# Kernel tuning notes

Hardware: AMD Instinct MI355X
Metric: run time of the kernel (lower is better)

Reference implementation:

```python
import jax, jax.numpy as jnp
from jax import lax
import numpy as np

EPS = 1e-5
SCALE, K_UP = 2, 5  # CARAFE defaults


def conv(x, w, pad=0):
    return lax.conv_general_dilated(x, w, (1, 1), [(pad, pad), (pad, pad)],
                                    dimension_numbers=('NCHW', 'OIHW', 'NCHW'))


def bn(x, g, b, m, v):
    # eval-mode BatchNorm2d
    inv = g * lax.rsqrt(v + EPS)
    return x * inv[None, :, None, None] + (b - m * inv)[None, :, None, None]


def carafe(X, comp_w, comp_g, comp_bt, comp_m, comp_v, enc_w, enc_g, enc_bt, enc_m, enc_v):
    b, c, h, w = X.shape
    k2 = K_UP * K_UP
    W = jax.nn.relu(bn(conv(X, comp_w), comp_g, comp_bt, comp_m, comp_v))  # (b, c_mid, h, w)
    W = bn(conv(W, enc_w, pad=1), enc_g, enc_bt, enc_m, enc_v)             # (b, k2*SCALE^2, h, w)
    # PixelShuffle(SCALE): (b, k2*r^2, h, w) -> (b, k2, h*r, w*r)
    W = W.reshape(b, k2, SCALE, SCALE, h, w).transpose(0, 1, 4, 2, 5, 3)
    W = W.reshape(b, k2, h * SCALE, w * SCALE)
    W = jax.nn.softmax(W, axis=1)
    # nearest upsample by SCALE
    Xu = jnp.repeat(jnp.repeat(X, SCALE, axis=2), SCALE, axis=3)
    pad = (K_UP // 2) * SCALE
    Xp = jnp.pad(Xu, ((0, 0), (0, 0), (pad, pad), (pad, pad)))
    h_, w_ = h * SCALE, w * SCALE
    # Unfold(kernel=K_UP, dilation=SCALE): channel-major then kernel index, matching torch
    patches = jnp.stack([Xp[:, :, i * SCALE:i * SCALE + h_, j * SCALE:j * SCALE + w_]
                         for i in range(K_UP) for j in range(K_UP)], axis=2)  # (b,c,k2,h_,w_)
    return jnp.einsum('bkhw,bckhw->bchw', W, patches)


def setup_inputs():
    key = jax.random.key(0)
    ks = iter(jax.random.split(key, 80))
    nk = lambda: next(ks)
    P = lambda shape, s=0.05: jax.random.normal(nk(), shape, jnp.float32) * s
    d = {}
    B, C_out = 4, 64
    cins = [128, 256, 512]
    hw = [(96, 160), (48, 80), (24, 40)]
    for i, (ci, (h, w)) in enumerate(zip(cins, hw)):
        d[f'x{i}'] = jax.random.normal(nk(), (B, ci, h, w), jnp.float32)
        d[f'lat{i}_w'] = P((C_out, ci, 1, 1))
        d[f'lat{i}_b'] = P((C_out,))
        d[f'fpn{i}_w'] = P((C_out, C_out, 3, 3))
        d[f'fpn{i}_b'] = P((C_out,))
    k2s2 = (SCALE * K_UP) ** 2
    for u in range(2):
        d[f'u{u}_comp_w'] = P((C_out, C_out, 1, 1))
        d[f'u{u}_enc_w'] = P((k2s2, C_out, 3, 3))
        for nm, c in [('comp', C_out), ('enc', k2s2)]:
            d[f'u{u}_{nm}_g'] = 1.0 + P((c,))
            d[f'u{u}_{nm}_bt'] = P((c,))
            d[f'u{u}_{nm}_m'] = P((c,))
            d[f'u{u}_{nm}_v'] = jax.random.uniform(nk(), (c,), jnp.float32, 0.5, 1.5)
    return d


def reference(x0, x1, x2,
              lat0_w, lat0_b, fpn0_w, fpn0_b,
              lat1_w, lat1_b, fpn1_w, fpn1_b,
              lat2_w, lat2_b, fpn2_w, fpn2_b,
              u0_comp_w, u0_enc_w, u0_comp_g, u0_comp_bt, u0_comp_m, u0_comp_v,
              u0_enc_g, u0_enc_bt, u0_enc_m, u0_enc_v,
              u1_comp_w, u1_enc_w, u1_comp_g, u1_comp_bt, u1_comp_m, u1_comp_v,
              u1_enc_g, u1_enc_bt, u1_enc_m, u1_enc_v):
    lat = [conv(x, w) + b[None, :, None, None] for x, w, b in
           [(x0, lat0_w, lat0_b), (x1, lat1_w, lat1_b), (x2, lat2_w, lat2_b)]]
    # top-down pathway with CARAFE upsampling
    lat[1] = lat[1] + carafe(lat[2], u1_comp_w, u1_comp_g, u1_comp_bt, u1_comp_m, u1_comp_v,
                             u1_enc_w, u1_enc_g, u1_enc_bt, u1_enc_m, u1_enc_v)
    lat[0] = lat[0] + carafe(lat[1], u0_comp_w, u0_comp_g, u0_comp_bt, u0_comp_m, u0_comp_v,
                             u0_enc_w, u0_enc_g, u0_enc_bt, u0_enc_m, u0_enc_v)
    outs = tuple(conv(l, w, pad=1) + b[None, :, None, None] for l, w, b in
                 [(lat[0], fpn0_w, fpn0_b), (lat[1], fpn1_w, fpn1_b), (lat[2], fpn2_w, fpn2_b)])
    return outs
```

## Files before the change

kernel.cpp:

```cpp
#include <hip/hip_runtime.h>

#define BN_EPS 1e-5f

typedef __attribute__((ext_vector_type(8))) short bf16x8;
typedef __attribute__((ext_vector_type(4))) float f32x4;

__device__ __forceinline__ unsigned short f2bf(float f) {
    unsigned u = __float_as_uint(f);
    return (unsigned short)((u + 0x7fffu + ((u >> 16) & 1u)) >> 16);
}
__device__ __forceinline__ unsigned packbf(float lo, float hi) {
    return ((unsigned)f2bf(hi) << 16) | (unsigned)f2bf(lo);
}

__global__ __launch_bounds__(256)
void prep_weights(const float* __restrict__ w0, const float* __restrict__ w1,
                  const float* __restrict__ w2, const float* __restrict__ w3,
                  const float* __restrict__ w4, unsigned short* __restrict__ dst,
                  const float* __restrict__ v0, const float* __restrict__ v1,
                  const float* __restrict__ v2, const float* __restrict__ v3,
                  const float* __restrict__ v4, unsigned short* __restrict__ dst1)
{
    int z = blockIdx.y;
    int i = blockIdx.x * 256 + threadIdx.x;
    if (z < 5) {
        const float* src; unsigned short* d; int C_out, COP;
        if (z < 3) {
            COP = 64; C_out = 64;
            src = (z == 0) ? w0 : (z == 1 ? w1 : w2);
            d = dst + z * 36864;
            if (i >= 36864) return;
        } else {
            COP = 112; C_out = 100;
            src = (z == 3) ? w3 : w4;
            d = dst + 110592 + (z - 3) * 64512;
            if (i >= 64512) return;
        }
        int tap = i / (COP * 64);
        int rem = i - tap * (COP * 64);
        int co = rem >> 6, ci = rem & 63;
        float v = (co < C_out) ? src[((size_t)co * 64 + ci) * 9 + tap] : 0.f;
        d[i] = f2bf(v);
    } else {
        int zz = z - 5;
        const float* s; int n; int off;
        if (zz == 0)      { s = v0; n = 8192;  off = 0; }
        else if (zz == 1) { s = v1; n = 16384; off = 8192; }
        else if (zz == 2) { s = v2; n = 32768; off = 24576; }
        else if (zz == 3) { s = v3; n = 4096;  off = 57344; }
        else              { s = v4; n = 4096;  off = 61440; }
        if (i >= n) return;
        dst1[off + i] = f2bf(s[i]);
    }
}

template<int COP, int CSPLIT, int MODE>
__device__ __forceinline__
void conv3x3_body(int rem, int TX, unsigned short* xs,
                  const unsigned* __restrict__ xp,
                  const unsigned short* __restrict__ wt,
                  const float* __restrict__ p0, const float* __restrict__ p1,
                  const float* __restrict__ p2, const float* __restrict__ p3,
                  float* __restrict__ out, int H, int W, int C_out)
{
    constexpr int NP = 324;
    constexpr int CT = COP / 16;
    static_assert(CT == CSPLIT, "CPB must be 1 (R1/R2 VGPR cliff)");

    int cs = rem % CSPLIT;
    int b  = (rem / CSPLIT) & 3;
    int t  = rem / (CSPLIT * 4);
    int x0 = (t % TX) * 16, y0 = (t / TX) * 16;

    int tid  = threadIdx.x;
    int lane = tid & 63, wid = tid >> 6;
    int lrow = lane >> 4, lcol = lane & 15;
    int HWp = H * W;

    int co0 = cs * 16;
    bool colok = (x0 + lcol) < W;

    f32x4 accA[2], accB[2];
#pragma unroll
    for (int rr = 0; rr < 2; ++rr) {
        accA[rr] = (f32x4){0.f, 0.f, 0.f, 0.f};
        accB[rr] = (f32x4){0.f, 0.f, 0.f, 0.f};
    }

    unsigned int* wsl = (unsigned int*)xs;

#pragma unroll 1
    for (int kb = 0; kb < 2; ++kb) {
        if (kb) __syncthreads();
        for (int p = tid; p < NP; p += 256) {
            int py = p / 18, px = p - py * 18;
            int gy = y0 + py - 1, gx = x0 + px - 1;
            bool ok = (gy >= 0) && (gy < H) && (gx >= 0) && (gx < W);
            const unsigned* gpp = xp + ((size_t)b * 32 + kb * 16) * HWp
                                     + (size_t)gy * W + gx;
#pragma unroll 8
            for (int cp = 0; cp < 16; ++cp) {
                unsigned pk = ok ? gpp[(size_t)cp * HWp] : 0u;
                wsl[((cp >> 2) * NP + p) * 4 + (cp & 3)] = pk;
            }
        }
        __syncthreads();

        bf16x8 a[9];
        const unsigned short* wl = wt + ((size_t)co0 + lcol) * 64 + kb * 32 + lrow * 8;
#pragma unroll
        for (int t9 = 0; t9 < 9; ++t9)
            a[t9] = *(const bf16x8*)(wl + (size_t)t9 * COP * 64);

#pragma unroll
        for (int rr = 0; rr < 2; ++rr) {
            int r0 = wid + rr * 8;
#pragma unroll
            for (int t9 = 0; t9 < 9; ++t9) {
                int dy = t9 / 3, dx = t9 - dy * 3;
                int g0 = lrow * NP + (r0 + dy) * 18 + lcol + dx;
                bf16x8 b0 = *(const bf16x8*)(xs + (size_t)g0 * 8);
                accA[rr] = __builtin_amdgcn_mfma_f32_16x16x32_bf16(a[t9], b0, accA[rr], 0, 0, 0);
                bf16x8 b1 = *(const bf16x8*)(xs + ((size_t)g0 + 4 * 18) * 8);
                accB[rr] = __builtin_amdgcn_mfma_f32_16x16x32_bf16(a[t9], b1, accB[rr], 0, 0, 0);
            }
        }
    }

    float sc[4], sh[4];
#pragma unroll
    for (int rg = 0; rg < 4; ++rg) {
        int co = co0 + lrow * 4 + rg;
        int cc = (co < C_out) ? co : 0;
        if (MODE == 0) { sc[rg] = 1.f; sh[rg] = p0[cc]; }
        else {
            float inv = p0[cc] * rsqrtf(p3[cc] + BN_EPS);
            sc[rg] = inv; sh[rg] = p1[cc] - p2[cc] * inv;
        }
    }
#pragma unroll
    for (int rr = 0; rr < 2; ++rr) {
        int r0 = wid + rr * 8;
        int yA = y0 + r0, yB = y0 + r0 + 4;
#pragma unroll
        for (int rg = 0; rg < 4; ++rg) {
            int co = co0 + lrow * 4 + rg;
            if (colok && co < C_out) {
                float* oc = out + (((size_t)b * C_out + co) * H) * W + x0 + lcol;
                if (yA < H) oc[(size_t)yA * W] = accA[rr][rg] * sc[rg] + sh[rg];
                if (yB < H) oc[(size_t)yB * W] = accB[rr][rg] * sc[rg] + sh[rg];
            }
        }
    }
}

__global__ __launch_bounds__(256, 6)
void enc_fpn(int encBlocks,
             const unsigned* __restrict__ cxp, const unsigned short* __restrict__ wt_e,
             const float* __restrict__ g, const float* __restrict__ bt,
             const float* __restrict__ m, const float* __restrict__ v,
             float* __restrict__ enc_out, int He, int We, int TXe,
             const unsigned* __restrict__ xp, const unsigned short* __restrict__ wt_f,
             const float* __restrict__ bias, float* __restrict__ fout,
             int Hf, int Wf, int TXf)
{
    __shared__ unsigned short xs[4 * 324 * 8];
    int f = blockIdx.x;
    if (f < encBlocks)
        conv3x3_body<112, 7, 1>(f, TXe, xs, cxp, wt_e,
                                g, bt, m, v, enc_out, He, We, 100);
    else
        conv3x3_body<64, 4, 0>(f - encBlocks, TXf, xs, xp, wt_f,
                               bias, nullptr, nullptr, nullptr, fout, Hf, Wf, 64);
}

__global__ __launch_bounds__(256, 6)
void fpn_multi(const unsigned* __restrict__ l0p, const unsigned short* __restrict__ wt0,
               const float* __restrict__ b0, float* __restrict__ o0)
{
    __shared__ unsigned short xs[4 * 324 * 8];
    conv3x3_body<64, 4, 0>(blockIdx.x, 10, xs, l0p, wt0,
                           b0, nullptr, nullptr, nullptr, o0, 96, 160, 64);
}

template<int C_IN, int NPX, int MODE, bool INPK, bool OUTMIR>
__device__ __forceinline__
void conv1x1_body(int f, unsigned short* xs,
                  const float* __restrict__ x, const unsigned* __restrict__ xp,
                  const unsigned short* __restrict__ wb,
                  const float* __restrict__ p0, const float* __restrict__ p1,
                  const float* __restrict__ p2, const float* __restrict__ p3,
                  float* __restrict__ out, unsigned* __restrict__ outp, int HW)
{
    constexpr int NT = NPX / 16;
    constexpr int QUADS = NPX / 4;
    int nb = HW / NPX;
    int px0 = (f % nb) * NPX;
    int b   = f / nb;

    int tid = threadIdx.x;
    int lane = tid & 63, wid = tid >> 6;
    int lrow = lane >> 4, lcol = lane & 15;
    const float*    xb  = INPK ? nullptr : x + (size_t)b * C_IN * HW + px0;
    const unsigned* xpb = INPK ? xp + (size_t)b * (C_IN / 2) * HW + px0 : nullptr;

    f32x4 acc[NT];
#pragma unroll
    for (int nt = 0; nt < NT; ++nt) acc[nt] = (f32x4){0.f, 0.f, 0.f, 0.f};

    for (int cc = 0; cc < C_IN; cc += 32) {
        if (cc) __syncthreads();
        for (int j = tid; j < 16 * QUADS; j += 256) {
            int q  = j & (QUADS - 1);
            int cp = j / QUADS;
            int px = q * 4;
            unsigned* wv = (unsigned*)xs + ((size_t)(cp >> 2) * NPX + px) * 4 + (cp & 3);
            if (INPK) {
                uint4 v = *(const uint4*)(xpb + (size_t)(cc / 2 + cp) * HW + px);
                wv[0] = v.x; wv[4] = v.y; wv[8] = v.z; wv[12] = v.w;
            } else {
                const float* s0 = xb + (size_t)(cc + 2 * cp) * HW + px;
                float4 v0 = *(const float4*)s0;
                float4 v1 = *(const float4*)(s0 + HW);
                wv[0]  = packbf(v0.x, v1.x);
                wv[4]  = packbf(v0.y, v1.y);
                wv[8]  = packbf(v0.z, v1.z);
                wv[12] = packbf(v0.w, v1.w);
            }
        }
        __syncthreads();

        bf16x8 a = *(const bf16x8*)(wb + (size_t)(wid * 16 + lcol) * C_IN + cc + lrow * 8);
#pragma unroll
        for (int nt = 0; nt < NT; ++nt) {
            bf16x8 bf = *(const bf16x8*)(xs + ((size_t)lrow * NPX + nt * 16 + lcol) * 8);
            acc[nt] = __builtin_amdgcn_mfma_f32_16x16x32_bf16(a, bf, acc[nt], 0, 0, 0);
        }
    }

    if (OUTMIR) {
#pragma unroll
        for (int rg = 0; rg < 4; rg += 2) {
            int co = wid * 16 + lrow * 4 + rg;
            float s0, h0, s1, h1;
            if (MODE == 0) { s0 = 1.f; h0 = p0[co]; s1 = 1.f; h1 = p0[co + 1]; }
            else {
                s0 = p0[co] * rsqrtf(p3[co] + BN_EPS);
                h0 = p1[co] - p2[co] * s0;
                s1 = p0[co + 1] * rsqrtf(p3[co + 1] + BN_EPS);
                h1 = p1[co + 1] - p2[co + 1] * s1;
            }
            unsigned* pp = outp + ((size_t)(b * 32 + (co >> 1))) * HW + px0;
#pragma unroll
            for (int nt = 0; nt < NT; ++nt) {
                float r0 = acc[nt][rg] * s0 + h0;
                float r1 = acc[nt][rg + 1] * s1 + h1;
                if (MODE == 1) { r0 = fmaxf(r0, 0.f); r1 = fmaxf(r1, 0.f); }
                pp[nt * 16 + lcol] = packbf(r0, r1);
            }
        }
    } else {
#pragma unroll
        for (int rg = 0; rg < 4; ++rg) {
            int co = wid * 16 + lrow * 4 + rg;
            float scale, shift;
            if (MODE == 0) { scale = 1.f; shift = p0[co]; }
            else {
                float inv = p0[co] * rsqrtf(p3[co] + BN_EPS);
                scale = inv; shift = p1[co] - p2[co] * inv;
            }
            float* op = out + ((size_t)(b * 64 + co)) * HW + px0;
#pragma unroll
            for (int nt = 0; nt < NT; ++nt) {
                float r = acc[nt][rg] * scale + shift;
                if (MODE == 1) r = fmaxf(r, 0.f);
                op[nt * 16 + lcol] = r;
            }
        }
    }
}

template<int C_IN, int NPX, int MODE, bool INPK, bool OUTMIR>
__global__ __launch_bounds__(256, 4)
void conv1x1_mfma(const float* __restrict__ x, const unsigned* __restrict__ xp,
                  const unsigned short* __restrict__ wb,
                  const float* __restrict__ p0, const float* __restrict__ p1,
                  const float* __restrict__ p2, const float* __restrict__ p3,
                  float* __restrict__ out, unsigned* __restrict__ outp, int HW)
{
    __shared__ __align__(16) unsigned short xs[4 * NPX * 8];
    int nb = HW / NPX;
    int f = blockIdx.x + nb * blockIdx.z;
    conv1x1_body<C_IN, NPX, MODE, INPK, OUTMIR>(f, xs, x, xp, wb, p0, p1, p2, p3, out, outp, HW);
}

__global__ __launch_bounds__(256, 4)
void lat_multi(const float* __restrict__ x0, const unsigned short* __restrict__ w0,
               const float* __restrict__ b0, float* __restrict__ lat0,
               const float* __restrict__ x1, const unsigned short* __restrict__ w1,
               const float* __restrict__ b1, float* __restrict__ lat1,
               const float* __restrict__ x2, const unsigned short* __restrict__ w2,
               const float* __restrict__ b2, unsigned* __restrict__ lat2p)
{
    __shared__ __align__(16) unsigned short xs[4 * 128 * 8];
    int f = blockIdx.x;
    if (f < 480)
        conv1x1_body<128, 128, 0, false, false>(f, xs, x0, nullptr, w0,
            b0, nullptr, nullptr, nullptr, lat0, nullptr, 15360);
    else if (f < 600)
        conv1x1_body<256, 128, 0, false, false>(f - 480, xs, x1, nullptr, w1,
            b1, nullptr, nullptr, nullptr, lat1, nullptr, 3840);
    else
        conv1x1_body<512, 64, 0, false, true>(f - 600, xs, x2, nullptr, w2,
            b2, nullptr, nullptr, nullptr, nullptr, lat2p, 960);
}

template<int CGS>
__global__ __launch_bounds__(256, 4)
void carafe_kernel(const unsigned* __restrict__ srcp, const float* __restrict__ logits,
                   const float* __restrict__ base, unsigned* __restrict__ dstp,
                   int h, int w)
{
    constexpr int SW = 12, NPX = 144;
    constexpr int CH = 64 / CGS;
    constexpr int CP = CH / 2;
    constexpr int CS = CH + 4;
    __shared__ float ls[NPX * CS];

    int tid = threadIdx.x;
    int x0 = blockIdx.x * 16, y0 = blockIdx.y * 16;
    int b  = blockIdx.z / CGS;
    int cs = blockIdx.z % CGS;
    int H = 2 * h, W = 2 * w;
    int xs0 = (x0 >> 1) - 2, ys0 = (y0 >> 1) - 2;
    size_t hw = (size_t)h * w;
    const unsigned* sb = srcp + ((size_t)(b * 32 + cs * CP)) * hw;

    for (int i = tid; i < NPX * CP; i += 256) {
        int cpl = i / NPX, p = i - cpl * NPX;
        int yy = p / SW, xx = p - yy * SW;
        int sy = ys0 + yy, sx = xs0 + xx;
        unsigned u = 0;
        if (sy >= 0 && sy < h && sx >= 0 && sx < w)
            u = sb[(size_t)cpl * hw + (size_t)sy * w + sx];
        ls[p * CS + 2 * cpl]     = __uint_as_float(u << 16);
        ls[p * CS + 2 * cpl + 1] = __uint_as_float(u & 0xffff0000u);
    }
    __syncthreads();

    int lx = tid & 15, ty = tid >> 4;
    int x = x0 + lx, y = y0 + ty;
    int xw = x >> 1, yh = y >> 1;
    int par = (y & 1) * 2 + (x & 1);

    const float* lp = logits + ((size_t)(b * 100 + par) * h + yh) * w + xw;
    float l[25];
    float mx = -1e30f;
#pragma unroll
    for (int k = 0; k < 25; ++k) {
        l[k] = lp[(size_t)(4 * k) * hw];
        mx = fmaxf(mx, l[k]);
    }
    float s = 0.f;
#pragma unroll
    for (int k = 0; k < 25; ++k) {
        l[k] = __expf(l[k] - mx);
        s += l[k];
    }
    float invs = 1.f / s;
#pragma unroll
    for (int k = 0; k < 25; ++k) l[k] *= invs;

    int pb = (yh - ys0 - 2) * SW + (xw - xs0 - 2);

#pragma unroll 1
    for (int cg = 0; cg < CH / 16; ++cg) {
        float acc[16];
#pragma unroll
        for (int c = 0; c < 16; ++c) acc[c] = 0.f;
#pragma unroll
        for (int k = 0; k < 25; ++k) {
            int ti = k / 5, tj = k - ti * 5;
            const float* q = &ls[(pb + ti * SW + tj) * CS + cg * 16];
            float wk = l[k];
#pragma unroll
            for (int c = 0; c < 16; ++c)
                acc[c] = fmaf(wk, q[c], acc[c]);
        }
        int cbase = cs * CH + cg * 16;
        const float* dp = base + (((size_t)(b * 64 + cbase)) * H + y) * W + x;
        unsigned* pp = dstp + (((size_t)(b * 32 + (cbase >> 1))) * H + y) * W + x;
#pragma unroll
        for (int c = 0; c < 16; c += 2) {
            float n0 = dp[(size_t)c * H * W] + acc[c];
            float n1 = dp[(size_t)(c + 1) * H * W] + acc[c + 1];
            pp[(size_t)(c >> 1) * H * W] = packbf(n0, n1);
        }
    }
}

extern "C" void kernel_launch(void* const* d_in, const int* in_sizes, int n_in,
                              void* d_out, int out_size, void* d_ws, size_t ws_size,
                              hipStream_t stream)
{
    const float* x0      = (const float*)d_in[0];
    const float* lat0_w  = (const float*)d_in[1];
    const float* lat0_b  = (const float*)d_in[2];
    const float* fpn0_w  = (const float*)d_in[3];
    const float* fpn0_b  = (const float*)d_in[4];
    const float* x1      = (const float*)d_in[5];
    const float* lat1_w  = (const float*)d_in[6];
    const float* lat1_b  = (const float*)d_in[7];
    const float* fpn1_w  = (const float*)d_in[8];
    const float* fpn1_b  = (const float*)d_in[9];
    const float* x2      = (const float*)d_in[10];
    const float* lat2_w  = (const float*)d_in[11];
    const float* lat2_b  = (const float*)d_in[12];
    const float* fpn2_w  = (const float*)d_in[13];
    const float* fpn2_b  = (const float*)d_in[14];
    const float* u0_comp_w = (const float*)d_in[15];
    const float* u0_enc_w  = (const float*)d_in[16];
    const float* u0_comp_g  = (const float*)d_in[17];
    const float* u0_comp_bt = (const float*)d_in[18];
    const float* u0_comp_m  = (const float*)d_in[19];
    const float* u0_comp_v  = (const float*)d_in[20];
    const float* u0_enc_g   = (const float*)d_in[21];
    const float* u0_enc_bt  = (const float*)d_in[22];
    const float* u0_enc_m   = (const float*)d_in[23];
    const float* u0_enc_v   = (const float*)d_in[24];
    const float* u1_comp_w = (const float*)d_in[25];
    const float* u1_enc_w  = (const float*)d_in[26];
    const float* u1_comp_g  = (const float*)d_in[27];
    const float* u1_comp_bt = (const float*)d_in[28];
    const float* u1_comp_m  = (const float*)d_in[29];
    const float* u1_comp_v  = (const float*)d_in[30];
    const float* u1_enc_g   = (const float*)d_in[31];
    const float* u1_enc_bt  = (const float*)d_in[32];
    const float* u1_enc_m   = (const float*)d_in[33];
    const float* u1_enc_v   = (const float*)d_in[34];

    float* out = (float*)d_out;
    const size_t OUT0 = 4ull * 64 * 96 * 160;
    const size_t OUT1 = 4ull * 64 * 48 * 80;
    const size_t OUT2 = 4ull * 64 * 24 * 40;
    float* out0 = out;
    float* out1 = out + OUT0;
    float* out2 = out + OUT0 + OUT1;

    float* lat0 = (float*)d_ws;
    float* lat1 = lat0 + OUT0;
    float* lat2 = lat1 + OUT1;
    unsigned short* wtb = (unsigned short*)(lat2 + OUT2);
    unsigned short* wt_fpn0 = wtb;
    unsigned short* wt_fpn1 = wtb + 36864;
    unsigned short* wt_fpn2 = wtb + 73728;
    unsigned short* wt_enc0 = wtb + 110592;
    unsigned short* wt_enc1 = wtb + 175104;
    unsigned short* wb = wtb + 239616;
    unsigned short* wb_lat0  = wb;
    unsigned short* wb_lat1  = wb + 8192;
    unsigned short* wb_lat2  = wb + 24576;
    unsigned short* wb_comp0 = wb + 57344;
    unsigned short* wb_comp1 = wb + 61440;
    unsigned* lat0p = (unsigned*)(wb + 65536);
    unsigned* lat1p = lat0p + 1966080;
    unsigned* lat2p = lat1p + 491520;
    unsigned* compp = lat2p + 122880;
    float* enc   = out0 + OUT1;

    dim3 blk(256);

    prep_weights<<<dim3(252, 10), blk, 0, stream>>>(
        fpn0_w, fpn1_w, fpn2_w, u0_enc_w, u1_enc_w, wtb,
        lat0_w, lat1_w, lat2_w, u0_comp_w, u1_comp_w, wb);

    lat_multi<<<dim3(660), blk, 0, stream>>>(
        x0, wb_lat0, lat0_b, lat0,
        x1, wb_lat1, lat1_b, lat1,
        x2, wb_lat2, lat2_b, lat2p);

    conv1x1_mfma<64, 32, 1, true, true><<<dim3(30, 1, 4), blk, 0, stream>>>(
        nullptr, lat2p, wb_comp1, u1_comp_g, u1_comp_bt, u1_comp_m, u1_comp_v,
        nullptr, compp, 24 * 40);
    enc_fpn<<<dim3(264), blk, 0, stream>>>(168,
        compp, wt_enc1, u1_enc_g, u1_enc_bt, u1_enc_m, u1_enc_v, enc, 24, 40, 3,
        lat2p, wt_fpn2, fpn2_b, out2, 24, 40, 3);
    carafe_kernel<2><<<dim3(5, 3, 8), blk, 0, stream>>>(lat2p, enc, lat1, lat1p, 24, 40);

    conv1x1_mfma<64, 32, 1, true, true><<<dim3(120, 1, 4), blk, 0, stream>>>(
        nullptr, lat1p, wb_comp0, u0_comp_g, u0_comp_bt, u0_comp_m, u0_comp_v,
        nullptr, compp, 48 * 80);
    enc_fpn<<<dim3(660), blk, 0, stream>>>(420,
        compp, wt_enc0, u0_enc_g, u0_enc_bt, u0_enc_m, u0_enc_v, enc, 48, 80, 5,
        lat1p, wt_fpn1, fpn1_b, out1, 48, 80, 5);
    carafe_kernel<2><<<dim3(10, 6, 8), blk, 0, stream>>>(lat1p, enc, lat0, lat0p, 48, 80);

    fpn_multi<<<dim3(960), blk, 0, stream>>>(lat0p, wt_fpn0, fpn0_b, out0);
}
```

Baseline: 276.2 us.

## Store lateral and encoder intermediates as bf16 and fold weight prep into lateral kernel

The lateral 1x1 conv outputs and the CARAFE encoder logits are now written as packed bf16 instead of fp32, and the CARAFE kernel reads them as bf16, which halves the intermediate memory traffic. The separate prep_weights launch is removed. 1x1 weights are converted from fp32 on the fly inside the MFMA loop, and the 3x3 weight repacking runs as extra blocks of the lateral kernel. This drops one kernel launch and several fp32 round trips. The cost is extra precision loss in the lateral sums and softmax logits, plus some repeated per-block weight conversion work.

```diff
diff --git a/kernel.cpp b/kernel.cpp
--- a/kernel.cpp
+++ b/kernel.cpp
@@ -12,56 +12,29 @@
 __device__ __forceinline__ unsigned packbf(float lo, float hi) {
     return ((unsigned)f2bf(hi) << 16) | (unsigned)f2bf(lo);
 }
-
-__global__ __launch_bounds__(256)
-void prep_weights(const float* __restrict__ w0, const float* __restrict__ w1,
-                  const float* __restrict__ w2, const float* __restrict__ w3,
-                  const float* __restrict__ w4, unsigned short* __restrict__ dst,
-                  const float* __restrict__ v0, const float* __restrict__ v1,
-                  const float* __restrict__ v2, const float* __restrict__ v3,
-                  const float* __restrict__ v4, unsigned short* __restrict__ dst1)
-{
-    int z = blockIdx.y;
-    int i = blockIdx.x * 256 + threadIdx.x;
-    if (z < 5) {
-        const float* src; unsigned short* d; int C_out, COP;
-        if (z < 3) {
-            COP = 64; C_out = 64;
-            src = (z == 0) ? w0 : (z == 1 ? w1 : w2);
-            d = dst + z * 36864;
-            if (i >= 36864) return;
-        } else {
-            COP = 112; C_out = 100;
-            src = (z == 3) ? w3 : w4;
-            d = dst + 110592 + (z - 3) * 64512;
-            if (i >= 64512) return;
-        }
-        int tap = i / (COP * 64);
-        int rem = i - tap * (COP * 64);
-        int co = rem >> 6, ci = rem & 63;
-        float v = (co < C_out) ? src[((size_t)co * 64 + ci) * 9 + tap] : 0.f;
-        d[i] = f2bf(v);
-    } else {
-        int zz = z - 5;
-        const float* s; int n; int off;
-        if (zz == 0)      { s = v0; n = 8192;  off = 0; }
-        else if (zz == 1) { s = v1; n = 16384; off = 8192; }
-        else if (zz == 2) { s = v2; n = 32768; off = 24576; }
-        else if (zz == 3) { s = v3; n = 4096;  off = 57344; }
-        else              { s = v4; n = 4096;  off = 61440; }
-        if (i >= n) return;
-        dst1[off + i] = f2bf(s[i]);
-    }
-}
-
-template<int COP, int CSPLIT, int MODE>
+__device__ __forceinline__ float bf2f(unsigned short u) {
+    return __uint_as_float((unsigned)u << 16);
+}
+__device__ __forceinline__ bf16x8 ldw8(const float* p) {
+    float4 a = *(const float4*)p;
+    float4 b = *(const float4*)(p + 4);
+    union { unsigned u[4]; bf16x8 v; } r;
+    r.u[0] = packbf(a.x, a.y);
+    r.u[1] = packbf(a.z, a.w);
+    r.u[2] = packbf(b.x, b.y);
+    r.u[3] = packbf(b.z, b.w);
+    return r.v;
+}
+
+template<int COP, int CSPLIT, int MODE, bool OBF16>
 __device__ __forceinline__
 void conv3x3_body(int rem, int TX, unsigned short* xs,
                   const unsigned* __restrict__ xp,
                   const unsigned short* __restrict__ wt,
                   const float* __restrict__ p0, const float* __restrict__ p1,
                   const float* __restrict__ p2, const float* __restrict__ p3,
-                  float* __restrict__ out, int H, int W, int C_out)
+                  float* __restrict__ out, unsigned short* __restrict__ out_us,
+                  int H, int W, int C_out)
 {
     constexpr int NP = 324;
     constexpr int CT = COP / 16;
@@ -146,9 +119,17 @@
         for (int rg = 0; rg < 4; ++rg) {
             int co = co0 + lrow * 4 + rg;
             if (colok && co < C_out) {
-                float* oc = out + (((size_t)b * C_out + co) * H) * W + x0 + lcol;
-                if (yA < H) oc[(size_t)yA * W] = accA[rr][rg] * sc[rg] + sh[rg];
-                if (yB < H) oc[(size_t)yB * W] = accB[rr][rg] * sc[rg] + sh[rg];
+                float vA = accA[rr][rg] * sc[rg] + sh[rg];
+                float vB = accB[rr][rg] * sc[rg] + sh[rg];
+                if (OBF16) {
+                    unsigned short* oc = out_us + (((size_t)b * C_out + co) * H) * W + x0 + lcol;
+                    if (yA < H) oc[(size_t)yA * W] = f2bf(vA);
+                    if (yB < H) oc[(size_t)yB * W] = f2bf(vB);
+                } else {
+                    float* oc = out + (((size_t)b * C_out + co) * H) * W + x0 + lcol;
+                    if (yA < H) oc[(size_t)yA * W] = vA;
+                    if (yB < H) oc[(size_t)yB * W] = vB;
+                }
             }
         }
     }
@@ -159,7 +140,7 @@
              const unsigned* __restrict__ cxp, const unsigned short* __restrict__ wt_e,
              const float* __restrict__ g, const float* __restrict__ bt,
              const float* __restrict__ m, const float* __restrict__ v,
-             float* __restrict__ enc_out, int He, int We, int TXe,
+             unsigned short* __restrict__ enc_us, int He, int We, int TXe,
              const unsigned* __restrict__ xp, const unsigned short* __restrict__ wt_f,
              const float* __restrict__ bias, float* __restrict__ fout,
              int Hf, int Wf, int TXf)
@@ -167,11 +148,11 @@
     __shared__ unsigned short xs[4 * 324 * 8];
     int f = blockIdx.x;
     if (f < encBlocks)
-        conv3x3_body<112, 7, 1>(f, TXe, xs, cxp, wt_e,
-                                g, bt, m, v, enc_out, He, We, 100);
+        conv3x3_body<112, 7, 1, true>(f, TXe, xs, cxp, wt_e,
+                                      g, bt, m, v, nullptr, enc_us, He, We, 100);
     else
-        conv3x3_body<64, 4, 0>(f - encBlocks, TXf, xs, xp, wt_f,
-                               bias, nullptr, nullptr, nullptr, fout, Hf, Wf, 64);
+        conv3x3_body<64, 4, 0, false>(f - encBlocks, TXf, xs, xp, wt_f,
+                                      bias, nullptr, nullptr, nullptr, fout, nullptr, Hf, Wf, 64);
 }
 
 __global__ __launch_bounds__(256, 6)
@@ -179,18 +160,18 @@
                const float* __restrict__ b0, float* __restrict__ o0)
 {
     __shared__ unsigned short xs[4 * 324 * 8];
-    conv3x3_body<64, 4, 0>(blockIdx.x, 10, xs, l0p, wt0,
-                           b0, nullptr, nullptr, nullptr, o0, 96, 160, 64);
-}
-
-template<int C_IN, int NPX, int MODE, bool INPK, bool OUTMIR>
+    conv3x3_body<64, 4, 0, false>(blockIdx.x, 10, xs, l0p, wt0,
+                                  b0, nullptr, nullptr, nullptr, o0, nullptr, 96, 160, 64);
+}
+
+template<int C_IN, int NPX, int MODE, bool INPK>
 __device__ __forceinline__
 void conv1x1_body(int f, unsigned short* xs,
                   const float* __restrict__ x, const unsigned* __restrict__ xp,
-                  const unsigned short* __restrict__ wb,
+                  const float* __restrict__ wf,
                   const float* __restrict__ p0, const float* __restrict__ p1,
                   const float* __restrict__ p2, const float* __restrict__ p3,
-                  float* __restrict__ out, unsigned* __restrict__ outp, int HW)
+                  unsigned* __restrict__ outp, int HW)
 {
     constexpr int NT = NPX / 16;
     constexpr int QUADS = NPX / 4;
@@ -230,7 +211,7 @@
         }
         __syncthreads();
 
-        bf16x8 a = *(const bf16x8*)(wb + (size_t)(wid * 16 + lcol) * C_IN + cc + lrow * 8);
+        bf16x8 a = ldw8(wf + (size_t)(wid * 16 + lcol) * C_IN + cc + lrow * 8);
 #pragma unroll
         for (int nt = 0; nt < NT; ++nt) {
             bf16x8 bf = *(const bf16x8*)(xs + ((size_t)lrow * NPX + nt * 16 + lcol) * 8);
@@ -238,87 +219,98 @@
         }
     }
 
-    if (OUTMIR) {
-#pragma unroll
-        for (int rg = 0; rg < 4; rg += 2) {
-            int co = wid * 16 + lrow * 4 + rg;
-            float s0, h0, s1, h1;
-            if (MODE == 0) { s0 = 1.f; h0 = p0[co]; s1 = 1.f; h1 = p0[co + 1]; }
-            else {
-                s0 = p0[co] * rsqrtf(p3[co] + BN_EPS);
-                h0 = p1[co] - p2[co] * s0;
-                s1 = p0[co + 1] * rsqrtf(p3[co + 1] + BN_EPS);
-                h1 = p1[co + 1] - p2[co + 1] * s1;
-            }
-            unsigned* pp = outp + ((size_t)(b * 32 + (co >> 1))) * HW + px0;
-#pragma unroll
-            for (int nt = 0; nt < NT; ++nt) {
-                float r0 = acc[nt][rg] * s0 + h0;
-                float r1 = acc[nt][rg + 1] * s1 + h1;
-                if (MODE == 1) { r0 = fmaxf(r0, 0.f); r1 = fmaxf(r1, 0.f); }
-                pp[nt * 16 + lcol] = packbf(r0, r1);
-            }
-        }
-    } else {
-#pragma unroll
-        for (int rg = 0; rg < 4; ++rg) {
-            int co = wid * 16 + lrow * 4 + rg;
-            float scale, shift;
-            if (MODE == 0) { scale = 1.f; shift = p0[co]; }
-            else {
-                float inv = p0[co] * rsqrtf(p3[co] + BN_EPS);
-                scale = inv; shift = p1[co] - p2[co] * inv;
-            }
-            float* op = out + ((size_t)(b * 64 + co)) * HW + px0;
-#pragma unroll
-            for (int nt = 0; nt < NT; ++nt) {
-                float r = acc[nt][rg] * scale + shift;
-                if (MODE == 1) r = fmaxf(r, 0.f);
-                op[nt * 16 + lcol] = r;
-            }
-        }
-    }
-}
-
-template<int C_IN, int NPX, int MODE, bool INPK, bool OUTMIR>
+#pragma unroll
+    for (int rg = 0; rg < 4; rg += 2) {
+        int co = wid * 16 + lrow * 4 + rg;
+        float s0, h0, s1, h1;
+        if (MODE == 0) { s0 = 1.f; h0 = p0[co]; s1 = 1.f; h1 = p0[co + 1]; }
+        else {
+            s0 = p0[co] * rsqrtf(p3[co] + BN_EPS);
+            h0 = p1[co] - p2[co] * s0;
+            s1 = p0[co + 1] * rsqrtf(p3[co + 1] + BN_EPS);
+            h1 = p1[co + 1] - p2[co + 1] * s1;
+        }
+        unsigned* pp = outp + ((size_t)(b * 32 + (co >> 1))) * HW + px0;
+#pragma unroll
+        for (int nt = 0; nt < NT; ++nt) {
+            float r0 = acc[nt][rg] * s0 + h0;
+            float r1 = acc[nt][rg + 1] * s1 + h1;
+            if (MODE == 1) { r0 = fmaxf(r0, 0.f); r1 = fmaxf(r1, 0.f); }
+            pp[nt * 16 + lcol] = packbf(r0, r1);
+        }
+    }
+}
+
+template<int C_IN, int NPX, int MODE, bool INPK>
 __global__ __launch_bounds__(256, 4)
 void conv1x1_mfma(const float* __restrict__ x, const unsigned* __restrict__ xp,
-                  const unsigned short* __restrict__ wb,
+                  const float* __restrict__ wf,
                   const float* __restrict__ p0, const float* __restrict__ p1,
                   const float* __restrict__ p2, const float* __restrict__ p3,
-                  float* __restrict__ out, unsigned* __restrict__ outp, int HW)
+                  unsigned* __restrict__ outp, int HW)
 {
     __shared__ __align__(16) unsigned short xs[4 * NPX * 8];
     int nb = HW / NPX;
     int f = blockIdx.x + nb * blockIdx.z;
-    conv1x1_body<C_IN, NPX, MODE, INPK, OUTMIR>(f, xs, x, xp, wb, p0, p1, p2, p3, out, outp, HW);
+    conv1x1_body<C_IN, NPX, MODE, INPK>(f, xs, x, xp, wf, p0, p1, p2, p3, outp, HW);
 }
 
 __global__ __launch_bounds__(256, 4)
-void lat_multi(const float* __restrict__ x0, const unsigned short* __restrict__ w0,
-               const float* __restrict__ b0, float* __restrict__ lat0,
-               const float* __restrict__ x1, const unsigned short* __restrict__ w1,
-               const float* __restrict__ b1, float* __restrict__ lat1,
-               const float* __restrict__ x2, const unsigned short* __restrict__ w2,
-               const float* __restrict__ b2, unsigned* __restrict__ lat2p)
+void lat_prep(const float* __restrict__ x0, const float* __restrict__ w0,
+              const float* __restrict__ b0, unsigned* __restrict__ lat0b,
+              const float* __restrict__ x1, const float* __restrict__ w1,
+              const float* __restrict__ b1, unsigned* __restrict__ lat1b,
+              const float* __restrict__ x2, const float* __restrict__ w2,
+              const float* __restrict__ b2, unsigned* __restrict__ lat2p,
+              const float* __restrict__ f0w, const float* __restrict__ f1w,
+              const float* __restrict__ f2w, const float* __restrict__ e0w,
+              const float* __restrict__ e1w, unsigned short* __restrict__ wtb)
 {
     __shared__ __align__(16) unsigned short xs[4 * 128 * 8];
     int f = blockIdx.x;
     if (f < 480)
-        conv1x1_body<128, 128, 0, false, false>(f, xs, x0, nullptr, w0,
-            b0, nullptr, nullptr, nullptr, lat0, nullptr, 15360);
+        conv1x1_body<128, 128, 0, false>(f, xs, x0, nullptr, w0,
+            b0, nullptr, nullptr, nullptr, lat0b, 15360);
     else if (f < 600)
-        conv1x1_body<256, 128, 0, false, false>(f - 480, xs, x1, nullptr, w1,
-            b1, nullptr, nullptr, nullptr, lat1, nullptr, 3840);
-    else
-        conv1x1_body<512, 64, 0, false, true>(f - 600, xs, x2, nullptr, w2,
-            b2, nullptr, nullptr, nullptr, nullptr, lat2p, 960);
+        conv1x1_body<256, 128, 0, false>(f - 480, xs, x1, nullptr, w1,
+            b1, nullptr, nullptr, nullptr, lat1b, 3840);
+    else if (f < 660)
+        conv1x1_body<512, 64, 0, false>(f - 600, xs, x2, nullptr, w2,
+            b2, nullptr, nullptr, nullptr, lat2p, 960);
+    else {
+        int base = (f - 660) * 1024 + threadIdx.x;
+#pragma unroll
+        for (int t = 0; t < 4; ++t) {
+            int i = base + t * 256;
+            float v;
+            if (i < 110592) {
+                int z = i / 36864;
+                int rem = i - z * 36864;
+                int tap = rem / 4096;
+                int r2 = rem - tap * 4096;
+                int co = r2 >> 6, ci = r2 & 63;
+                const float* src = (z == 0) ? f0w : (z == 1 ? f1w : f2w);
+                v = src[((size_t)co * 64 + ci) * 9 + tap];
+            } else {
+                int j = i - 110592;
+                int z = j / 64512;
+                int rem = j - z * 64512;
+                int tap = rem / 7168;
+                int r2 = rem - tap * 7168;
+                int co = r2 >> 6, ci = r2 & 63;
+                const float* src = z ? e1w : e0w;
+                v = (co < 100) ? src[((size_t)co * 64 + ci) * 9 + tap] : 0.f;
+            }
+            wtb[i] = f2bf(v);
+        }
+    }
 }
 
 template<int CGS>
 __global__ __launch_bounds__(256, 4)
-void carafe_kernel(const unsigned* __restrict__ srcp, const float* __restrict__ logits,
-                   const float* __restrict__ base, unsigned* __restrict__ dstp,
+void carafe_kernel(const unsigned* __restrict__ srcp,
+                   const unsigned short* __restrict__ logits_us,
+                   const unsigned* __restrict__ basep, unsigned* __restrict__ dstp,
                    int h, int w)
 {
     constexpr int SW = 12, NPX = 144;
@@ -353,12 +345,12 @@
     int xw = x >> 1, yh = y >> 1;
     int par = (y & 1) * 2 + (x & 1);
 
-    const float* lp = logits + ((size_t)(b * 100 + par) * h + yh) * w + xw;
+    const unsigned short* lp = logits_us + ((size_t)(b * 100 + par) * h + yh) * w + xw;
     float l[25];
     float mx = -1e30f;
 #pragma unroll
     for (int k = 0; k < 25; ++k) {
-        l[k] = lp[(size_t)(4 * k) * hw];
+        l[k] = bf2f(lp[(size_t)(4 * k) * hw]);
         mx = fmaxf(mx, l[k]);
     }
     float s = 0.f;
@@ -388,12 +380,14 @@
                 acc[c] = fmaf(wk, q[c], acc[c]);
         }
         int cbase = cs * CH + cg * 16;
-        const float* dp = base + (((size_t)(b * 64 + cbase)) * H + y) * W + x;
-        unsigned* pp = dstp + (((size_t)(b * 32 + (cbase >> 1))) * H + y) * W + x;
+        size_t poff = (((size_t)(b * 32 + (cbase >> 1))) * H + y) * W + x;
+        const unsigned* bp = basep + poff;
+        unsigned* pp = dstp + poff;
 #pragma unroll
         for (int c = 0; c < 16; c += 2) {
-            float n0 = dp[(size_t)c * H * W] + acc[c];
-            float n1 = dp[(size_t)(c + 1) * H * W] + acc[c + 1];
+            unsigned ub = bp[(size_t)(c >> 1) * H * W];
+            float n0 = __uint_as_float(ub << 16) + acc[c];
+            float n1 = __uint_as_float(ub & 0xffff0000u) + acc[c + 1];
             pp[(size_t)(c >> 1) * H * W] = packbf(n0, n1);
         }
     }
@@ -447,53 +441,43 @@
     float* out1 = out + OUT0;
     float* out2 = out + OUT0 + OUT1;
 
-    float* lat0 = (float*)d_ws;
-    float* lat1 = lat0 + OUT0;
-    float* lat2 = lat1 + OUT1;
-    unsigned short* wtb = (unsigned short*)(lat2 + OUT2);
+    unsigned* lat0b = (unsigned*)d_ws;
+    unsigned* lat1b = lat0b + 1966080;
+    unsigned short* wtb = (unsigned short*)(lat1b + 491520);
     unsigned short* wt_fpn0 = wtb;
     unsigned short* wt_fpn1 = wtb + 36864;
     unsigned short* wt_fpn2 = wtb + 73728;
     unsigned short* wt_enc0 = wtb + 110592;
     unsigned short* wt_enc1 = wtb + 175104;
-    unsigned short* wb = wtb + 239616;
-    unsigned short* wb_lat0  = wb;
-    unsigned short* wb_lat1  = wb + 8192;
-    unsigned short* wb_lat2  = wb + 24576;
-    unsigned short* wb_comp0 = wb + 57344;
-    unsigned short* wb_comp1 = wb + 61440;
-    unsigned* lat0p = (unsigned*)(wb + 65536);
+    unsigned* lat0p = (unsigned*)(wtb + 239616);
     unsigned* lat1p = lat0p + 1966080;
     unsigned* lat2p = lat1p + 491520;
     unsigned* compp = lat2p + 122880;
-    float* enc   = out0 + OUT1;
+    unsigned short* enc_us = (unsigned short*)(out0 + OUT1);
 
     dim3 blk(256);
 
-    prep_weights<<<dim3(252, 10), blk, 0, stream>>>(
-        fpn0_w, fpn1_w, fpn2_w, u0_enc_w, u1_enc_w, wtb,
-        lat0_w, lat1_w, lat2_w, u0_comp_w, u1_comp_w, wb);
-
-    lat_multi<<<dim3(660), blk, 0, stream>>>(
-        x0, wb_lat0, lat0_b, lat0,
-        x1, wb_lat1, lat1_b, lat1,
-        x2, wb_lat2, lat2_b, lat2p);
-
-    conv1x1_mfma<64, 32, 1, true, true><<<dim3(30, 1, 4), blk, 0, stream>>>(
-        nullptr, lat2p, wb_comp1, u1_comp_g, u1_comp_bt, u1_comp_m, u1_comp_v,
-        nullptr, compp, 24 * 40);
+    lat_prep<<<dim3(894), blk, 0, stream>>>(
+        x0, lat0_w, lat0_b, lat0b,
+        x1, lat1_w, lat1_b, lat1b,
+        x2, lat2_w, lat2_b, lat2p,
+        fpn0_w, fpn1_w, fpn2_w, u0_enc_w, u1_enc_w, wtb);
+
+    conv1x1_mfma<64, 32, 1, true><<<dim3(30, 1, 4), blk, 0, stream>>>(
+        nullptr, lat2p, u1_comp_w, u1_comp_g, u1_comp_bt, u1_comp_m, u1_comp_v,
+        compp, 24 * 40);
     enc_fpn<<<dim3(264), blk, 0, stream>>>(168,
-        compp, wt_enc1, u1_enc_g, u1_enc_bt, u1_enc_m, u1_enc_v, enc, 24, 40, 3,
+        compp, wt_enc1, u1_enc_g, u1_enc_bt, u1_enc_m, u1_enc_v, enc_us, 24, 40, 3,
         lat2p, wt_fpn2, fpn2_b, out2, 24, 40, 3);
-    carafe_kernel<2><<<dim3(5, 3, 8), blk, 0, stream>>>(lat2p, enc, lat1, lat1p, 24, 40);
-
-    conv1x1_mfma<64, 32, 1, true, true><<<dim3(120, 1, 4), blk, 0, stream>>>(
-        nullptr, lat1p, wb_comp0, u0_comp_g, u0_comp_bt, u0_comp_m, u0_comp_v,
-        nullptr, compp, 48 * 80);
+    carafe_kernel<2><<<dim3(5, 3, 8), blk, 0, stream>>>(lat2p, enc_us, lat1b, lat1p, 24, 40);
+
+    conv1x1_mfma<64, 32, 1, true><<<dim3(120, 1, 4), blk, 0, stream>>>(
+        nullptr, lat1p, u0_comp_w, u0_comp_g, u0_comp_bt, u0_comp_m, u0_comp_v,
+        compp, 48 * 80);
     enc_fpn<<<dim3(660), blk, 0, stream>>>(420,
-        compp, wt_enc0, u0_enc_g, u0_enc_bt, u0_enc_m, u0_enc_v, enc, 48, 80, 5,
+        compp, wt_enc0, u0_enc_g, u0_enc_bt, u0_enc_m, u0_enc_v, enc_us, 48, 80, 5,
         lat1p, wt_fpn1, fpn1_b, out1, 48, 80, 5);
-    carafe_kernel<2><<<dim3(10, 6, 8), blk, 0, stream>>>(lat1p, enc, lat0, lat0p, 48, 80);
+    carafe_kernel<2><<<dim3(10, 6, 8), blk, 0, stream>>>(lat1p, enc_us, lat0b, lat0p, 48, 80);
 
     fpn_multi<<<dim3(960), blk, 0, stream>>>(lat0p, wt_fpn0, fpn0_b, out0);
 }
```

Measured after the change: 272.4 us. No clear change (-1.4%).
